# Kernel tuning notes

Hardware: AMD Instinct MI355X
Metric: run time of the kernel (lower is better)

Reference implementation:

```python
import jax, jax.numpy as jnp
import numpy as np

T, B, S, V = 50, 64, 400, 50000
D = 512; E = 512; H = 512; A = 512; POOL = 2


def setup_inputs() -> dict:
    key = jax.random.key(0)
    ks = jax.random.split(key, 20)
    def rn(k, shape, s=0.05):
        return jax.random.normal(k, shape, jnp.float32) * s
    return {
        "input_y": jax.random.randint(ks[0], (T, B), 0, V),
        "hidden": rn(ks[1], (1, B, H), 1.0),
        "context": rn(ks[2], (S, B, E), 1.0),
        "src_pad_mask": jnp.zeros((B, S), jnp.float32),
        "init_att": rn(ks[3], (B, E), 1.0),
        "coverage": jnp.zeros((B, S), jnp.float32),
        "global_ctx": rn(ks[4], (B, E), 1.0),
        "emb_W": rn(ks[5], (V, D)).at[0].set(0.0),  # padding_idx=0
        "W_ih": rn(ks[6], (3 * H, D + E)),
        "W_hh": rn(ks[7], (3 * H, H)),
        "b_ih": jnp.zeros((3 * H,), jnp.float32),
        "b_hh": jnp.zeros((3 * H,), jnp.float32),
        "W_pre": rn(ks[8], (E, A)),
        "b_pre": jnp.zeros((A,), jnp.float32),
        "W_q": rn(ks[9], (H + E, A)),
        "W_v": rn(ks[10], (A,)),
        "W_cov": rn(ks[11], (A,)),
        "W_pgen": rn(ks[12], (E + H + D,)),
        "b_pgen": jnp.zeros((), jnp.float32),
        "W_ro": rn(ks[13], (D + H + E + E, H)),
        "b_ro": jnp.zeros((H,), jnp.float32),
    }


def _gru_cell(x, h, W_ih, W_hh, b_ih, b_hh):
    # PyTorch GRUCell gate order: r, z, n
    gi = x @ W_ih.T + b_ih
    gh = h @ W_hh.T + b_hh
    i_r, i_z, i_n = jnp.split(gi, 3, axis=-1)
    h_r, h_z, h_n = jnp.split(gh, 3, axis=-1)
    r = jax.nn.sigmoid(i_r + h_r)
    z = jax.nn.sigmoid(i_z + h_z)
    n = jnp.tanh(i_n + r * h_n)
    return (1.0 - z) * n + z * h


def reference(input_y, hidden, context, src_pad_mask, init_att, coverage, global_ctx,
              emb_W, W_ih, W_hh, b_ih, b_hh, W_pre, b_pre, W_q, W_v, W_cov,
              W_pgen, b_pgen, W_ro, b_ro):
    emb = emb_W[input_y]                      # [T,B,D]
    ctx = jnp.transpose(context, (1, 0, 2))   # [B,S,E]
    precompute = ctx @ W_pre + b_pre          # [B,S,A] (computed once, as in module)
    pad = src_pad_mask > 0.5
    NEG = jnp.float32(-1e18)

    def step(carry, emb_t):
        h, cur_ctx, cov = carry
        x = jnp.concatenate([emb_t, cur_ctx], 1)          # input feed
        h0 = _gru_cell(x, h[0], W_ih, W_hh, b_ih, b_hh)   # layers=1
        h = h.at[0].set(h0)
        output = h0
        # concat attention with coverage
        q = jnp.concatenate([output, global_ctx], 1) @ W_q          # [B,A]
        tmp = jnp.tanh(precompute + q[:, None, :] + cov[..., None] * W_cov)
        energy = tmp @ W_v                                           # [B,S]
        energy = jnp.where(pad, NEG, energy)
        attn = jax.nn.softmax(energy, axis=1)
        cur_ctx = jnp.einsum('bs,bse->be', attn, ctx)
        # pointer-gen
        p_gen = jax.nn.sigmoid(
            jnp.concatenate([cur_ctx, output, emb_t], 1) @ W_pgen + b_pgen)[:, None]
        # readout + maxout (dropout is identity in eval)
        readout = jnp.concatenate([emb_t, output, cur_ctx, global_ctx], 1) @ W_ro + b_ro
        mo = readout.reshape(B, H // POOL, POOL).max(axis=-1)        # [B,H/POOL]
        cov_loss = jnp.sum(jnp.minimum(attn, cov), 1)                # cov_loss_wt=1.0
        next_cov = cov + attn
        return (h, cur_ctx, next_cov), (mo, p_gen, attn, cov_loss)

    (hidden_f, cur_ctx_f, cov_f), (g_out, g_pg, g_attn, cov_losses) = jax.lax.scan(
        step, (hidden, init_att, coverage), emb)
    return (g_out, hidden_f, g_attn[-1], cur_ctx_f, g_pg, g_attn, cov_losses, cov_f)
```

## Files before the change

### kernel.cpp

```cpp
#include <hip/hip_runtime.h>
#include <hip/hip_bf16.h>


#define T_STEPS 50
#define BB 64
#define SS 400

#define O_GOUT 0
#define O_HID 819200
#define O_ATTN_LAST 851968
#define O_CTXF 877568
#define O_PG 910336
#define O_GATTN 913536
#define O_COVL 2193536
#define O_COVF 2196736

typedef __attribute__((ext_vector_type(4))) float f4;
typedef __attribute__((ext_vector_type(8))) short s8v;
typedef __attribute__((ext_vector_type(4))) unsigned u4;
typedef unsigned long long u64;

static __device__ __forceinline__ float bf2f(unsigned short u){
  unsigned v = ((unsigned)u) << 16; return __builtin_bit_cast(float, v);
}
static __device__ __forceinline__ unsigned short f2bf(float f){
  unsigned u = __builtin_bit_cast(unsigned, f);
  unsigned r = (u + 0x7FFFu + ((u >> 16) & 1u)) >> 16;
  return (unsigned short)r;
}
static __device__ __forceinline__ float sigmoidf_(float x){ return 1.f/(1.f+__expf(-x)); }
static __device__ __forceinline__ float tanhf_(float x){ float e=__expf(2.f*x); return 1.f - 2.f/(e+1.f); }
static __device__ __forceinline__ float ald32f(const float* p){
  unsigned u = __hip_atomic_load((const unsigned*)p, __ATOMIC_RELAXED, __HIP_MEMORY_SCOPE_AGENT);
  return __builtin_bit_cast(float, u);
}
static __device__ __forceinline__ void ast32f(float* p, float v){
  __hip_atomic_store((unsigned*)p, __builtin_bit_cast(unsigned, v),
                     __ATOMIC_RELAXED, __HIP_MEMORY_SCOPE_AGENT);
}
static __device__ __forceinline__ u64 ald64(const void* p){
  return __hip_atomic_load((const u64*)p, __ATOMIC_RELAXED, __HIP_MEMORY_SCOPE_AGENT);
}
static __device__ __forceinline__ void ast64(void* p, u64 v){
  __hip_atomic_store((u64*)p, v, __ATOMIC_RELAXED, __HIP_MEMORY_SCOPE_AGENT);
}

__global__ void conv_ctx(const float* __restrict__ ctx, unsigned short* __restrict__ out){
  int o = blockIdx.x*256 + threadIdx.x;
  if(o >= SS*BB*512) return;
  int e = o & 511; int b = (o>>9)&63; int s = o>>15;
  out[((b*SS+s)<<9) + e] = f2bf(ctx[o]);
}
__global__ void conv_emb(const int* __restrict__ y, const float* __restrict__ embW,
                         unsigned short* __restrict__ embU){
  int o = blockIdx.x*256+threadIdx.x; if(o>=T_STEPS*BB*512) return;
  int d = o & 511; int i = o>>9;
  embU[o] = f2bf(embW[(long)y[i]*512 + d]);
}
__global__ void conv_rest(const float* __restrict__ W_ih, const float* __restrict__ W_hh,
                          const float* __restrict__ W_pre, const float* __restrict__ W_ro,
                          const float* __restrict__ W_q,
                          const float* __restrict__ hidden, const float* __restrict__ init_att,
                          const float* __restrict__ gctx, const float* __restrict__ coverage,
                          unsigned short* __restrict__ wihbf, unsigned short* __restrict__ wpreT,
                          unsigned short* __restrict__ wroT, unsigned short* __restrict__ Wgru,
                          unsigned short* __restrict__ WqP,
                          float* __restrict__ hrow0, unsigned short* __restrict__ h0bf_init,
                          unsigned short* __restrict__ ctx0bf, float* __restrict__ gctxT,
                          float* __restrict__ cov, unsigned* __restrict__ flags){
  int o = blockIdx.x*256+threadIdx.x;
  if(o < 786432){
    int j = o>>9; int d = o&511;
    wihbf[o] = f2bf(W_ih[(long)j*1024 + d]);
  } else if(o < 1048576){
    int p = o - 786432;
    int a = p>>9; int e = p&511;
    wpreT[p] = f2bf(W_pre[(long)e*512 + a]);
  } else if(o < 2097152){
    int p = o - 1048576;
    int n = p>>11; int k = p&2047;
    wroT[p] = f2bf(W_ro[(long)k*512 + n]);
  } else if(o < 3670016){
    int p = o - 2097152;
    int rg = p >> 13; int rem = p & 8191;
    int ki = rem >> 9; int ln = (rem >> 3) & 63; int e = p & 7;
    int blk = rg/24; int r2 = rg%24; int w = r2/6; int r3 = r2%6; int g = r3>>1; int op = r3&1;
    int rl = ln & 15; int kk = ((ln>>4)<<3) + e;
    int d = blk*64 + w*16 + rl; int j = g*512 + d; int k = ki*32 + kk;
    float v = op ? W_hh[(long)j*512 + k] : W_ih[(long)j*1024 + 512 + k];
    Wgru[p] = f2bf(v);
  } else if(o < 3932160){
    int p = o - 3670016;
    int e = p&7; int ln=(p>>3)&63; int kf=(p>>9)&1; int nrg=(p>>10)&31; int blk=p>>15;
    int n = nrg*16 + (ln&15);
    int k = blk*64 + kf*32 + ((ln>>4)<<3) + e;
    WqP[p] = f2bf(W_q[(long)k*512 + n]);
  } else if(o < 4056192){
    int p = o - 3932160;
    if(p < 32768){ float v = hidden[p]; hrow0[p] = v; h0bf_init[p] = f2bf(v); }
    else if(p < 65536){ int q=p-32768; ctx0bf[q] = f2bf(init_att[q]); }
    else if(p < 98304){ int q=p-65536; int b=q>>9,e=q&511; gctxT[e*64+b]=gctx[q]; }
    else if(p < 123904){ int q=p-98304; cov[q]=coverage[q]; }
    else { int q=p-123904; if(q<128) flags[q]=0u; }
  }
}

template<int OUT_BF16>
__global__ __launch_bounds__(256) void mfma_gemm(
    const unsigned short* __restrict__ Abf, int lda,
    const unsigned short* __restrict__ Bbf, int ldb,
    void* __restrict__ Cp, int ldc, const float* __restrict__ bias, int K)
{
  __shared__ __align__(16) unsigned short Ash[128*40];
  __shared__ __align__(16) unsigned short Bsh[128*40];
  int m0 = blockIdx.x*128, n0 = blockIdx.y*128;
  int tid = threadIdx.x;
  int wid = tid>>6, lane = tid&63;
  int wm = wid>>1, wn = wid&1;
  int lr = lane&15, lg = lane>>4;
  f4 acc[4][4];
  #pragma unroll
  for(int i=0;i<4;i++)
    #pragma unroll
    for(int j=0;j<4;j++) acc[i][j]=(f4)0.f;

  for(int kt=0; kt<K; kt+=32){
    #pragma unroll
    for(int c=0;c<2;c++){
      int flat = tid*16 + c*8;
      int row = flat>>5, col = flat&31;
      const unsigned short* ga = Abf + (long)(m0+row)*lda + kt + col;
      *(uint4*)(&Ash[row*40+col]) = *(const uint4*)ga;
      const unsigned short* gb = Bbf + (long)(n0+row)*ldb + kt + col;
      *(uint4*)(&Bsh[row*40+col]) = *(const uint4*)gb;
    }
    __syncthreads();
    s8v av[4], bv[4];
    #pragma unroll
    for(int mi=0;mi<4;mi++) av[mi] = *(const s8v*)(&Ash[(wm*64+mi*16+lr)*40 + lg*8]);
    #pragma unroll
    for(int ni=0;ni<4;ni++) bv[ni] = *(const s8v*)(&Bsh[(wn*64+ni*16+lr)*40 + lg*8]);
    #pragma unroll
    for(int mi=0;mi<4;mi++)
      #pragma unroll
      for(int ni=0;ni<4;ni++)
        acc[mi][ni] = __builtin_amdgcn_mfma_f32_16x16x32_bf16(av[mi], bv[ni], acc[mi][ni], 0,0,0);
    __syncthreads();
  }
  #pragma unroll
  for(int mi=0;mi<4;mi++)
    #pragma unroll
    for(int ni=0;ni<4;ni++){
      int gc = n0 + wn*64 + ni*16 + lr;
      #pragma unroll
      for(int r=0;r<4;r++){
        int gr = m0 + wm*64 + mi*16 + lg*4 + r;
        float v = acc[mi][ni][r];
        if(bias) v += bias[gc];
        if(OUT_BF16) ((unsigned short*)Cp)[(long)gr*ldc + gc] = f2bf(v);
        else         ((float*)Cp)[(long)gr*ldc + gc] = v;
      }
    }
}

__global__ __launch_bounds__(256) void mfma_gemm_ro(
    const unsigned short* __restrict__ embU, const unsigned short* __restrict__ h0bf,
    const unsigned short* __restrict__ ctxA, const unsigned short* __restrict__ wroT,
    float* __restrict__ RO, const float* __restrict__ bias)
{
  __shared__ __align__(16) unsigned short Ash[128*40];
  __shared__ __align__(16) unsigned short Bsh[128*40];
  int m0 = blockIdx.x*128, n0 = blockIdx.y*128;
  int tid = threadIdx.x;
  int wid = tid>>6, lane = tid&63;
  int wm = wid>>1, wn = wid&1;
  int lr = lane&15, lg = lane>>4;
  f4 acc[4][4];
  #pragma unroll
  for(int i=0;i<4;i++)
    #pragma unroll
    for(int j=0;j<4;j++) acc[i][j]=(f4)0.f;

  for(int kt=0; kt<1536; kt+=32){
    const unsigned short* src = (kt<512) ? embU : (kt<1024) ? h0bf : ctxA;
    int klocal = kt & 511;
    #pragma unroll
    for(int c=0;c<2;c++){
      int flat = tid*16 + c*8;
      int row = flat>>5, col = flat&31;
      *(uint4*)(&Ash[row*40+col]) = *(const uint4*)(src + (long)(m0+row)*512 + klocal + col);
      *(uint4*)(&Bsh[row*40+col]) = *(const uint4*)(wroT + (long)(n0+row)*2048 + kt + col);
    }
    __syncthreads();
    s8v av[4], bv[4];
    #pragma unroll
    for(int mi=0;mi<4;mi++) av[mi] = *(const s8v*)(&Ash[(wm*64+mi*16+lr)*40 + lg*8]);
    #pragma unroll
    for(int ni=0;ni<4;ni++) bv[ni] = *(const s8v*)(&Bsh[(wn*64+ni*16+lr)*40 + lg*8]);
    #pragma unroll
    for(int mi=0;mi<4;mi++)
      #pragma unroll
      for(int ni=0;ni<4;ni++)
        acc[mi][ni] = __builtin_amdgcn_mfma_f32_16x16x32_bf16(av[mi], bv[ni], acc[mi][ni], 0,0,0);
    __syncthreads();
  }
  #pragma unroll
  for(int mi=0;mi<4;mi++)
    #pragma unroll
    for(int ni=0;ni<4;ni++){
      int gc = n0 + wn*64 + ni*16 + lr;
      #pragma unroll
      for(int r=0;r<4;r++){
        int gr = m0 + wm*64 + mi*16 + lg*4 + r;
        RO[(long)gr*512 + gc] = acc[mi][ni][r] + bias[gc];
      }
    }
}

__global__ __launch_bounds__(256) void small2(
  const float* __restrict__ AT, const float* __restrict__ W_q, const float* __restrict__ W_ro,
  float* __restrict__ q_g, float* __restrict__ ro_g)
{
  int blk = blockIdx.x;
  int half = blk>>7; int nblk = blk&127;
  int tid = threadIdx.x;
  int b = tid&63; int nq = tid>>6;
  int n = __builtin_amdgcn_readfirstlane(nblk*4 + nq);
  const float* W = half ? W_ro : W_q;
  int koff = half ? 1536 : 512;
  float acc = 0.f;
  const float* wp = W + (long)koff*512 + n;
  #pragma unroll 8
  for(int k=0;k<512;k++){
    acc = fmaf(AT[k*64+b], wp[(long)k*512], acc);
  }
  (half ? ro_g : q_g)[b*512+n] = acc;
}

__global__ __launch_bounds__(512) void k_step(
  const unsigned short* __restrict__ ctx0bf, float* __restrict__ ctxP,
  float* __restrict__ S_part, float* __restrict__ P_exp,
  const unsigned short* __restrict__ hprevbf,
  const float* __restrict__ hrow_in, float* __restrict__ hrow_out,
  const unsigned short* __restrict__ Wp, const unsigned short* __restrict__ WqP,
  const float* __restrict__ gi_emb, const float* __restrict__ b_hh,
  unsigned short* __restrict__ h0bf_all, float* __restrict__ qpart,
  float* __restrict__ cov, unsigned short* __restrict__ ctxA,
  unsigned short* __restrict__ ctxR,
  const unsigned short* __restrict__ pre, const unsigned short* __restrict__ ctxbf,
  const float* __restrict__ q_g, const float* __restrict__ Wv,
  const float* __restrict__ Wcov, const float* __restrict__ padm,
  float* __restrict__ covl_part, unsigned* __restrict__ flags,
  float* __restrict__ outp, int t)
{
  __shared__ __align__(16) char smem[75008];
  const int blk = blockIdx.x;
  const int tid = threadIdx.x;
  const int w = tid>>6, lane = tid&63;
  const int lr = lane&15, lg = lane>>4;

  if(blk < 64){
    if(t==0) return;
    int b = blk; int tb = t-1;
    if(tid < 128){
      const float* Sp = S_part + (tb&1)*256 + b*4;
      float inv = 1.f/(Sp[0]+Sp[1]+Sp[2]+Sp[3]);
      int e0 = tid*4;
      const float* cp = ctxP + (long)b*2048 + e0;
      f4 p0 = *(const f4*)cp;
      f4 p1 = *(const f4*)(cp+512);
      f4 p2 = *(const f4*)(cp+1024);
      f4 p3 = *(const f4*)(cp+1536);
      f4 s = (p0+p1+p2+p3)*inv;
      u64 v = (u64)f2bf(s.x) | ((u64)f2bf(s.y)<<16) | ((u64)f2bf(s.z)<<32) | ((u64)f2bf(s.w)<<48);
      ast64(ctxR + b*512 + e0, v);
      *(u64*)(ctxA + (long)(tb*64+b)*512 + e0) = v;
    }
    asm volatile("s_waitcnt vmcnt(0)" ::: "memory");
    __syncthreads();
    if(tid==0)
      __hip_atomic_fetch_add(flags+64+t, 1u, __ATOMIC_RELEASE, __HIP_MEMORY_SCOPE_AGENT);
    return;
  }

  if(blk < 72){
    int gblk = blk - 64;
    unsigned short* Ash = (unsigned short*)smem;
    unsigned short* HS  = (unsigned short*)(smem+65536);
    const int swz = (lr&7)<<4;
    const int dg = w&3, bh = w>>2;
    const int rgbase = gblk*24 + dg*6;

    if(t>0){
      if(tid==0){
        unsigned it=0;
        while(__hip_atomic_load(flags+64+t, __ATOMIC_RELAXED, __HIP_MEMORY_SCOPE_AGENT) < 64u){
          __builtin_amdgcn_s_sleep(2);
          if(++it > 20000000u) break;
        }
      }
      __syncthreads();
      asm volatile("" ::: "memory");
    }

    f4 acc2[6][2];
    #pragma unroll
    for(int u=0;u<6;u++)
      #pragma unroll
      for(int mm=0;mm<2;mm++) acc2[u][mm]=(f4)0.f;

    for(int kp=0; kp<2; kp++){
      for(int c = tid; c < 4096; c += 512){
        int op = c>>11; int row = (c>>5)&63; int kc = c&31;
        int e0 = kp*256 + kc*8;
        u4 v;
        if(op){
          v = *(const u4*)(hprevbf + row*512 + e0);
        } else if(t>0){
          u64 lo = ald64(ctxR + row*512 + e0);
          u64 hi = ald64(ctxR + row*512 + e0 + 4);
          v.x = (unsigned)lo; v.y = (unsigned)(lo>>32);
          v.z = (unsigned)hi; v.w = (unsigned)(hi>>32);
        } else {
          v = *(const u4*)(ctx0bf + row*512 + e0);
        }
        int dst = op*32768 + row*512 + ((kc*16) ^ ((row&7)<<4));
        *(u4*)((char*)Ash + dst) = v;
      }
      __syncthreads();
      {
        #pragma unroll 2
        for(int ktl=0; ktl<256; ktl+=32){
          s8v av[2][2];
          #pragma unroll
          for(int op=0;op<2;op++)
            #pragma unroll
            for(int mm=0;mm<2;mm++){
              int mi = bh*2+mm;
              av[op][mm] = *(const s8v*)((const char*)Ash + op*32768 + (mi*16+lr)*512 + ((ktl*2 + lg*16) ^ swz));
            }
          int ki = kp*8 + (ktl>>5);
          const unsigned short* wb = Wp + (long)rgbase*8192 + ki*512 + lane*8;
          #pragma unroll
          for(int u=0;u<6;u++){
            s8v bv = *(const s8v*)(wb + (long)u*8192);
            #pragma unroll
            for(int mm=0;mm<2;mm++)
              acc2[u][mm] = __builtin_amdgcn_mfma_f32_16x16x32_bf16(av[u&1][mm], bv, acc2[u][mm], 0,0,0);
          }
        }
      }
      __syncthreads();
    }

    {
      int d = gblk*64 + dg*16 + lr;
      float bhr = b_hh[d], bhz = b_hh[512+d], bhn = b_hh[1024+d];
      #pragma unroll
      for(int mm=0;mm<2;mm++){
        int mi = bh*2+mm;
        #pragma unroll
        for(int r=0;r<4;r++){
          int b = mi*16 + lg*4 + r;
          const float* ge = gi_emb + (long)(t*64+b)*1536;
          float g0 = __builtin_nontemporal_load(ge + d);
          float g1 = __builtin_nontemporal_load(ge + 512 + d);
          float g2 = __builtin_nontemporal_load(ge + 1024 + d);
          float rr = sigmoidf_(g0 + bhr + acc2[0][mm][r] + acc2[1][mm][r]);
          float zz = sigmoidf_(g1 + bhz + acc2[2][mm][r] + acc2[3][mm][r]);
          float nn = tanhf_(  g2       + acc2[4][mm][r] + rr*(acc2[5][mm][r] + bhn));
          float hp = hrow_in[b*512 + d];
          float hv = (1.f-zz)*nn + zz*hp;
          hrow_out[b*512+d] = hv;
          unsigned short hb = f2bf(hv);
          h0bf_all[(long)(t*64+b)*512 + d] = hb;
          HS[b*72 + dg*16 + lr] = hb;
          if(t==T_STEPS-1) outp[O_HID + b*512 + d] = hv;
        }
      }
    }
    __syncthreads();
    {
      #pragma unroll
      for(int i=0;i<8;i++){
        f4 accq[2];
        accq[0]=(f4)0.f; accq[1]=(f4)0.f;
        #pragma unroll
        for(int kf=0;kf<2;kf++){
          s8v bv = *(const s8v*)(WqP + ((((long)gblk*32 + (dg*8+i))*2 + kf)*64 + lane)*8);
          #pragma unroll
          for(int mm=0;mm<2;mm++){
            int mi = bh*2+mm;
            s8v av = *(const s8v*)(HS + (mi*16+lr)*72 + kf*32 + lg*8);
            accq[mm] = __builtin_amdgcn_mfma_f32_16x16x32_bf16(av, bv, accq[mm], 0,0,0);
          }
        }
        int n = dg*128 + i*16 + lr;
        #pragma unroll
        for(int mm=0;mm<2;mm++)
          #pragma unroll
          for(int r=0;r<4;r++)
            ast32f(qpart + (long)gblk*32768 + (long)((bh*2+mm)*16+lg*4+r)*512 + n, accq[mm][r]);
      }
    }
    asm volatile("s_waitcnt vmcnt(0)" ::: "memory");
    __syncthreads();
    if(tid==0)
      __hip_atomic_fetch_add(flags+t, 1u, __ATOMIC_RELEASE, __HIP_MEMORY_SCOPE_AGENT);
    return;
  }

  {
    int eb = blk-72; int b = eb>>2, cq = eb&3, c0 = cq*100;
    float* q_sh  = (float*)smem;
    float* wv_sh = (float*)(smem+2048);
    float* wc_sh = (float*)(smem+4096);
    float* covL  = (float*)(smem+6144);
    float* padL  = (float*)(smem+6560);
    float* red   = (float*)(smem+7392);
    float* red2  = (float*)(smem+9440);
    float* pb    = (float*)(smem+9472);

    wv_sh[tid]=Wv[tid]; wc_sh[tid]=Wcov[tid];
    if(tid<100) padL[tid]=padm[b*400+c0+tid];
    float clp = 0.f;
    if(t>0){
      const float* Sp = S_part + ((t-1)&1)*256 + b*4;
      float inv = 1.f/(Sp[0]+Sp[1]+Sp[2]+Sp[3]);
      if(tid<100){
        float p = P_exp[b*400+c0+tid]*inv;
        float co = cov[b*400+c0+tid];
        clp = fminf(p,co);
        float nc = co+p;
        cov[b*400+c0+tid]=nc;
        covL[tid]=nc;
        outp[O_GATTN + (long)(t-1)*25600 + b*400 + c0 + tid] = p;
      }
    } else {
      if(tid<100) covL[tid]=cov[b*400+c0+tid];
    }
    const unsigned short* prow = pre   + (((long)(b*400+c0))<<9) + lane*8;
    const unsigned short* crow = ctxbf + (((long)(b*400+c0))<<9) + lane*8;
    u4 pr[13], cr[13];
    #pragma unroll
    for(int j=0;j<13;j++){
      int i = w + j*8;
      long ro = (long)((i<100)? i : 0) << 9;
      pr[j] = *(const u4*)(prow + ro);
      cr[j] = *(const u4*)(crow + ro);
    }
    red[tid]=clp; __syncthreads();
    for(int o=256;o;o>>=1){ if(tid<o) red[tid]+=red[tid+o]; __syncthreads(); }
    if(t>0 && tid==0) covl_part[(long)(t-1)*256 + b*4+cq] = red[0];
    if(tid==0){
      unsigned it=0;
      while(__hip_atomic_load(flags+t, __ATOMIC_RELAXED, __HIP_MEMORY_SCOPE_AGENT) < 8u){
        __builtin_amdgcn_s_sleep(8);
        if(++it > 20000000u) break;
      }
    }
    __syncthreads();
    asm volatile("" ::: "memory");
    {
      float acc = q_g[b*512+tid];
      #pragma unroll
      for(int p=0;p<8;p++) acc += ald32f(qpart + ((long)p<<15) + b*512 + tid);
      q_sh[tid] = acc;
    }
    __syncthreads();
    float wsum = 0.f;
    float acc8[8];
    #pragma unroll
    for(int j=0;j<8;j++) acc8[j]=0.f;
    #pragma unroll
    for(int j=0;j<13;j++){
      int i = w + j*8;
      if(i<100){
        u4 cur = pr[j];
        const unsigned* uu = (const unsigned*)&cur;
        float cv = covL[i];
        float part = 0.f;
        #pragma unroll
        for(int q4=0;q4<4;q4++){
          int a = lane*8 + q4*2;
          part += wv_sh[a]  * tanhf_(bf2f((unsigned short)(uu[q4]&0xffffu)) + q_sh[a]   + cv*wc_sh[a]);
          part += wv_sh[a+1]* tanhf_(bf2f((unsigned short)(uu[q4]>>16))    + q_sh[a+1] + cv*wc_sh[a+1]);
        }
        #pragma unroll
        for(int off=32;off;off>>=1) part += __shfl_xor(part, off, 64);
        float e = (padL[i]>0.5f) ? -1e18f : part;
        float p = __expf(e);
        if(lane==0) P_exp[b*400+c0+i] = p;
        wsum += p;
        u4 cc = cr[j];
        const unsigned* cu = (const unsigned*)&cc;
        acc8[0] = fmaf(p, bf2f((unsigned short)(cu[0]&0xffffu)), acc8[0]);
        acc8[1] = fmaf(p, bf2f((unsigned short)(cu[0]>>16)),     acc8[1]);
        acc8[2] = fmaf(p, bf2f((unsigned short)(cu[1]&0xffffu)), acc8[2]);
        acc8[3] = fmaf(p, bf2f((unsigned short)(cu[1]>>16)),     acc8[3]);
        acc8[4] = fmaf(p, bf2f((unsigned short)(cu[2]&0xffffu)), acc8[4]);
        acc8[5] = fmaf(p, bf2f((unsigned short)(cu[2]>>16)),     acc8[5]);
        acc8[6] = fmaf(p, bf2f((unsigned short)(cu[3]&0xffffu)), acc8[6]);
        acc8[7] = fmaf(p, bf2f((unsigned short)(cu[3]>>16)),     acc8[7]);
      }
    }
    if(lane==0) red2[w]=wsum;
    __syncthreads();
    if(tid==0)
      S_part[(t&1)*256 + b*4+cq] = red2[0]+red2[1]+red2[2]+red2[3]+red2[4]+red2[5]+red2[6]+red2[7];
    #pragma unroll
    for(int j=0;j<8;j++) pb[w*512 + lane*8+j] = acc8[j];
    __syncthreads();
    {
      float v = pb[tid]+pb[512+tid]+pb[1024+tid]+pb[1536+tid]
               +pb[2048+tid]+pb[2560+tid]+pb[3072+tid]+pb[3584+tid];
      ctxP[((long)b*4+cq)*512 + tid] = v;
    }
  }
}

__global__ __launch_bounds__(256) void k_fin(
  const float* __restrict__ ctxP, const float* __restrict__ S_part,
  const float* __restrict__ P_exp, const float* __restrict__ cov,
  const float* __restrict__ covl_part,
  unsigned short* __restrict__ ctxA, float* __restrict__ outp)
{
  __shared__ float red[256];
  int b = blockIdx.x; int tid = threadIdx.x;
  const int tb = T_STEPS-1;
  const float* Sp = S_part + 256 + b*4;
  float S = Sp[0]+Sp[1]+Sp[2]+Sp[3];
  float inv = 1.f/S;
  float clp;
  {
    float p = P_exp[b*400+tid]*inv;
    float co = cov[b*400+tid];
    clp = fminf(p, co);
    float nc = co+p;
    outp[O_GATTN + (long)tb*25600 + b*400 + tid] = p;
    outp[O_ATTN_LAST + b*400 + tid] = p;
    outp[O_COVF + b*400 + tid] = nc;
  }
  if(tid<144){
    int i = 256+tid;
    float p = P_exp[b*400+i]*inv;
    float co = cov[b*400+i];
    clp += fminf(p, co);
    float nc = co+p;
    outp[O_GATTN + (long)tb*25600 + b*400 + i] = p;
    outp[O_ATTN_LAST + b*400 + i] = p;
    outp[O_COVF + b*400 + i] = nc;
  }
  red[tid]=clp; __syncthreads();
  for(int o=128;o;o>>=1){ if(tid<o) red[tid]+=red[tid+o]; __syncthreads(); }
  if(tid==0) outp[O_COVL + tb*64 + b] = red[0];
  if(tid<49){
    const float* cp = covl_part + (long)tid*256 + b*4;
    outp[O_COVL + tid*64 + b] = cp[0]+cp[1]+cp[2]+cp[3];
  }
  for(int c=tid;c<512;c+=256){
    float v = (ctxP[(long)b*2048+c]+ctxP[(long)b*2048+512+c]
              +ctxP[(long)b*2048+1024+c]+ctxP[(long)b*2048+1536+c])*inv;
    outp[O_CTXF + b*512 + c] = v;
    ctxA[(long)(tb*64+b)*512 + c] = f2bf(v);
  }
}

__global__ __launch_bounds__(256) void k_post(
  const unsigned short* __restrict__ embU, const unsigned short* __restrict__ h0bf,
  const unsigned short* __restrict__ ctxA, const float* __restrict__ Wpg,
  const float* __restrict__ bpg, const float* __restrict__ RO,
  const float* __restrict__ ro_g, float* __restrict__ outp)
{
  int blk = blockIdx.x;
  if(blk < 800){
    int wid = threadIdx.x>>6, lane=threadIdx.x&63;
    int m = blk*4 + wid;
    float acc=0.f;
    #pragma unroll
    for(int i=0;i<8;i++){
      int k = i*64+lane;
      acc = fmaf(bf2f(ctxA[(long)m*512+k]), Wpg[k], acc);
      acc = fmaf(bf2f(h0bf[(long)m*512+k]), Wpg[512+k], acc);
      acc = fmaf(bf2f(embU[(long)m*512+k]), Wpg[1024+k], acc);
    }
    #pragma unroll
    for(int off=32; off; off>>=1) acc += __shfl_xor(acc, off, 64);
    if(lane==0) outp[O_PG + m] = sigmoidf_(acc + bpg[0]);
  } else {
    int o = (blk-800)*256 + threadIdx.x;
    int h = o & 255; int m = o>>8; int b = m & 63;
    float v0 = RO[(long)m*512 + 2*h]   + ro_g[b*512 + 2*h];
    float v1 = RO[(long)m*512 + 2*h+1] + ro_g[b*512 + 2*h+1];
    outp[O_GOUT + o] = fmaxf(v0,v1);
  }
}

extern "C" void kernel_launch(void* const* d_in, const int* in_sizes, int n_in,
                              void* d_out, int out_size, void* d_ws, size_t ws_size,
                              hipStream_t stream)
{
  (void)in_sizes; (void)n_in; (void)out_size; (void)ws_size;
  const int*   y       = (const int*)d_in[0];
  const float* hidden  = (const float*)d_in[1];
  const float* context = (const float*)d_in[2];
  const float* padm    = (const float*)d_in[3];
  const float* init_att= (const float*)d_in[4];
  const float* coverage= (const float*)d_in[5];
  const float* gctx    = (const float*)d_in[6];
  const float* embW    = (const float*)d_in[7];
  const float* W_ih    = (const float*)d_in[8];
  const float* W_hh    = (const float*)d_in[9];
  const float* b_ih    = (const float*)d_in[10];
  const float* b_hh    = (const float*)d_in[11];
  const float* W_pre   = (const float*)d_in[12];
  const float* b_pre   = (const float*)d_in[13];
  const float* W_q     = (const float*)d_in[14];
  const float* W_v     = (const float*)d_in[15];
  const float* W_cov   = (const float*)d_in[16];
  const float* W_pg    = (const float*)d_in[17];
  const float* b_pg    = (const float*)d_in[18];
  const float* W_ro    = (const float*)d_in[19];
  const float* b_ro    = (const float*)d_in[20];
  float* out = (float*)d_out;

  char* wsb = (char*)d_ws;
  size_t off = 0;
  auto alloc = [&](size_t bytes)->char*{ char* p = wsb+off; off += (bytes+255)&~255UL; return p; };
  unsigned short* pre    = (unsigned short*)alloc(25600UL*512*2);
  unsigned short* ctxbf  = (unsigned short*)alloc(13107200UL*2);
  unsigned short* embU   = (unsigned short*)alloc(3200UL*512*2);
  unsigned short* wihbf  = (unsigned short*)alloc(1536UL*512*2);
  unsigned short* wpreT  = (unsigned short*)alloc(512UL*512*2);
  unsigned short* wroT   = (unsigned short*)alloc(512UL*2048*2);
  unsigned short* Wgru   = (unsigned short*)alloc(192UL*8192*2);
  unsigned short* WqP    = (unsigned short*)alloc(262144UL*2);
  float* gi_emb = (float*)alloc(3200UL*1536*4);
  float* RO     = (float*)alloc(3200UL*512*4);
  float* q_g    = (float*)alloc(64UL*512*4);
  float* ro_g   = (float*)alloc(64UL*512*4);
  float* hrow0  = (float*)alloc(64UL*512*4);
  float* hrow1  = (float*)alloc(64UL*512*4);
  float* gctxT  = (float*)alloc(512UL*64*4);
  unsigned short* h0bf = (unsigned short*)alloc(3200UL*512*2);
  unsigned short* h0bf_init = (unsigned short*)alloc(64UL*512*2);
  unsigned short* ctx0bf    = (unsigned short*)alloc(64UL*512*2);
  unsigned short* ctxA = (unsigned short*)alloc(3200UL*512*2);
  unsigned short* ctxR = (unsigned short*)alloc(64UL*512*2);
  float* ctxP   = (float*)alloc(64UL*4*512*4);
  float* P_exp  = (float*)alloc(64UL*400*4);
  float* S_part = (float*)alloc(2UL*256*4);
  float* qpart  = (float*)alloc(8UL*64*512*4);
  float* cov    = (float*)alloc(64UL*400*4);
  float* covl_part = (float*)alloc(50UL*256*4);
  unsigned* flags = (unsigned*)alloc(128UL*4);

  conv_ctx <<<dim3(51200),dim3(256),0,stream>>>(context, ctxbf);
  conv_emb <<<dim3(6400), dim3(256),0,stream>>>(y, embW, embU);
  conv_rest<<<dim3(15845),dim3(256),0,stream>>>(W_ih, W_hh, W_pre, W_ro, W_q,
                                                hidden, init_att, gctx, coverage,
                                                wihbf, wpreT, wroT, Wgru, WqP,
                                                hrow0, h0bf_init, ctx0bf, gctxT, cov, flags);

  mfma_gemm<1><<<dim3(200,4),dim3(256),0,stream>>>(ctxbf,512, wpreT,512,  pre,   512, b_pre, 512);
  mfma_gemm<0><<<dim3(25,12),dim3(256),0,stream>>>(embU, 512, wihbf,512,  gi_emb,1536, b_ih, 512);
  small2<<<dim3(256),dim3(256),0,stream>>>(gctxT, W_q, W_ro, q_g, ro_g);

  for(int t=0; t<T_STEPS; t++){
    float* hin  = (t&1) ? hrow1 : hrow0;
    float* hout = (t&1) ? hrow0 : hrow1;
    const unsigned short* hprevbf = t ? (h0bf + (long)(t-1)*32768) : h0bf_init;
    k_step<<<dim3(328),dim3(512),0,stream>>>(ctx0bf, ctxP, S_part, P_exp, hprevbf,
                                             hin, hout, Wgru, WqP, gi_emb, b_hh,
                                             h0bf, qpart, cov, ctxA, ctxR, pre, ctxbf,
                                             q_g, W_v, W_cov, padm, covl_part,
                                             flags, out, t);
  }

  k_fin<<<dim3(64),dim3(256),0,stream>>>(ctxP, S_part, P_exp, cov, covl_part, ctxA, out);
  mfma_gemm_ro<<<dim3(25,4),dim3(256),0,stream>>>(embU, h0bf, ctxA, wroT, RO, b_ro);
  k_post<<<dim3(4000),dim3(256),0,stream>>>(embU, h0bf, ctxA, W_pg, b_pg, RO, ro_g, out);
}
```

Before: 2.759 ms.

## Precompute next step's hidden-state GRU GEMM after publishing h, off critical path

The GRU blocks now split the recurrent GEMM. The W_hh·h part for step t+1 is computed at the end of step t, right after all 8 GRU blocks have published h through a new exchange buffer hX. It is stored in gh_buf, so at step t+1 only the context-dependent W_ih·ctx half has to run after waiting on the attention context. This takes about half the GRU matmul work off the critical dependency on the previous step's attention. It adds an inter-block spin wait among the GRU blocks and extra global traffic. Separately, the three conversion kernels are merged into one launch.

```diff
diff --git a/kernel.cpp b/kernel.cpp
--- a/kernel.cpp
+++ b/kernel.cpp
@@ -45,30 +45,33 @@
   __hip_atomic_store((u64*)p, v, __ATOMIC_RELAXED, __HIP_MEMORY_SCOPE_AGENT);
 }
 
-__global__ void conv_ctx(const float* __restrict__ ctx, unsigned short* __restrict__ out){
+__global__ void conv_all(const float* __restrict__ ctx, const int* __restrict__ y,
+                         const float* __restrict__ embW,
+                         const float* __restrict__ W_ih, const float* __restrict__ W_hh,
+                         const float* __restrict__ W_pre, const float* __restrict__ W_ro,
+                         const float* __restrict__ W_q,
+                         const float* __restrict__ hidden, const float* __restrict__ init_att,
+                         const float* __restrict__ gctx, const float* __restrict__ coverage,
+                         unsigned short* __restrict__ ctxbf, unsigned short* __restrict__ embU,
+                         unsigned short* __restrict__ wihbf, unsigned short* __restrict__ wpreT,
+                         unsigned short* __restrict__ wroT, unsigned short* __restrict__ Wgru,
+                         unsigned short* __restrict__ WqP,
+                         float* __restrict__ hrow0, unsigned short* __restrict__ h0bf_init,
+                         unsigned short* __restrict__ ctx0bf, float* __restrict__ gctxT,
+                         float* __restrict__ cov, unsigned* __restrict__ flags){
   int o = blockIdx.x*256 + threadIdx.x;
-  if(o >= SS*BB*512) return;
-  int e = o & 511; int b = (o>>9)&63; int s = o>>15;
-  out[((b*SS+s)<<9) + e] = f2bf(ctx[o]);
-}
-__global__ void conv_emb(const int* __restrict__ y, const float* __restrict__ embW,
-                         unsigned short* __restrict__ embU){
-  int o = blockIdx.x*256+threadIdx.x; if(o>=T_STEPS*BB*512) return;
-  int d = o & 511; int i = o>>9;
-  embU[o] = f2bf(embW[(long)y[i]*512 + d]);
-}
-__global__ void conv_rest(const float* __restrict__ W_ih, const float* __restrict__ W_hh,
-                          const float* __restrict__ W_pre, const float* __restrict__ W_ro,
-                          const float* __restrict__ W_q,
-                          const float* __restrict__ hidden, const float* __restrict__ init_att,
-                          const float* __restrict__ gctx, const float* __restrict__ coverage,
-                          unsigned short* __restrict__ wihbf, unsigned short* __restrict__ wpreT,
-                          unsigned short* __restrict__ wroT, unsigned short* __restrict__ Wgru,
-                          unsigned short* __restrict__ WqP,
-                          float* __restrict__ hrow0, unsigned short* __restrict__ h0bf_init,
-                          unsigned short* __restrict__ ctx0bf, float* __restrict__ gctxT,
-                          float* __restrict__ cov, unsigned* __restrict__ flags){
-  int o = blockIdx.x*256+threadIdx.x;
+  if(o < 13107200){
+    int e = o & 511; int b = (o>>9)&63; int s = o>>15;
+    ctxbf[((b*SS+s)<<9) + e] = f2bf(ctx[o]);
+    return;
+  }
+  o -= 13107200;
+  if(o < 1638400){
+    int d = o & 511; int i = o>>9;
+    embU[o] = f2bf(embW[(long)y[i]*512 + d]);
+    return;
+  }
+  o -= 1638400;
   if(o < 786432){
     int j = o>>9; int d = o&511;
     wihbf[o] = f2bf(W_ih[(long)j*1024 + d]);
@@ -240,13 +243,14 @@
 __global__ __launch_bounds__(512) void k_step(
   const unsigned short* __restrict__ ctx0bf, float* __restrict__ ctxP,
   float* __restrict__ S_part, float* __restrict__ P_exp,
-  const unsigned short* __restrict__ hprevbf,
+  const unsigned short* __restrict__ h0bf_init,
   const float* __restrict__ hrow_in, float* __restrict__ hrow_out,
   const unsigned short* __restrict__ Wp, const unsigned short* __restrict__ WqP,
   const float* __restrict__ gi_emb, const float* __restrict__ b_hh,
   unsigned short* __restrict__ h0bf_all, float* __restrict__ qpart,
   float* __restrict__ cov, unsigned short* __restrict__ ctxA,
-  unsigned short* __restrict__ ctxR,
+  unsigned short* __restrict__ ctxR, unsigned short* __restrict__ hX,
+  float* __restrict__ gh_buf,
   const unsigned short* __restrict__ pre, const unsigned short* __restrict__ ctxbf,
   const float* __restrict__ q_g, const float* __restrict__ Wv,
   const float* __restrict__ Wcov, const float* __restrict__ padm,
@@ -287,48 +291,26 @@
     int gblk = blk - 64;
     unsigned short* Ash = (unsigned short*)smem;
     unsigned short* HS  = (unsigned short*)(smem+65536);
+    char* ash_b = (char*)Ash;
     const int swz = (lr&7)<<4;
     const int dg = w&3, bh = w>>2;
     const int rgbase = gblk*24 + dg*6;
-
-    if(t>0){
-      if(tid==0){
-        unsigned it=0;
-        while(__hip_atomic_load(flags+64+t, __ATOMIC_RELAXED, __HIP_MEMORY_SCOPE_AGENT) < 64u){
-          __builtin_amdgcn_s_sleep(2);
-          if(++it > 20000000u) break;
-        }
-      }
-      __syncthreads();
-      asm volatile("" ::: "memory");
-    }
-
-    f4 acc2[6][2];
-    #pragma unroll
-    for(int u=0;u<6;u++)
-      #pragma unroll
-      for(int mm=0;mm<2;mm++) acc2[u][mm]=(f4)0.f;
-
-    for(int kp=0; kp<2; kp++){
-      for(int c = tid; c < 4096; c += 512){
-        int op = c>>11; int row = (c>>5)&63; int kc = c&31;
-        int e0 = kp*256 + kc*8;
-        u4 v;
-        if(op){
-          v = *(const u4*)(hprevbf + row*512 + e0);
-        } else if(t>0){
-          u64 lo = ald64(ctxR + row*512 + e0);
-          u64 hi = ald64(ctxR + row*512 + e0 + 4);
-          v.x = (unsigned)lo; v.y = (unsigned)(lo>>32);
-          v.z = (unsigned)hi; v.w = (unsigned)(hi>>32);
-        } else {
-          v = *(const u4*)(ctx0bf + row*512 + e0);
-        }
-        int dst = op*32768 + row*512 + ((kc*16) ^ ((row&7)<<4));
-        *(u4*)((char*)Ash + dst) = v;
-      }
-      __syncthreads();
-      {
+    const int d = gblk*64 + dg*16 + lr;
+
+    if(t==0){
+      f4 acc2[6][2];
+      #pragma unroll
+      for(int u=0;u<6;u++){ acc2[u][0]=(f4)0.f; acc2[u][1]=(f4)0.f; }
+      for(int kp=0; kp<2; kp++){
+        for(int c = tid; c < 4096; c += 512){
+          int op = c>>11; int row = (c>>5)&63; int kc = c&31;
+          int e0 = kp*256 + kc*8;
+          u4 v = op ? *(const u4*)(h0bf_init + row*512 + e0)
+                    : *(const u4*)(ctx0bf + row*512 + e0);
+          int dst = op*32768 + row*512 + ((kc*16) ^ ((row&7)<<4));
+          *(u4*)(ash_b + dst) = v;
+        }
+        __syncthreads();
         #pragma unroll 2
         for(int ktl=0; ktl<256; ktl+=32){
           s8v av[2][2];
@@ -337,7 +319,7 @@
             #pragma unroll
             for(int mm=0;mm<2;mm++){
               int mi = bh*2+mm;
-              av[op][mm] = *(const s8v*)((const char*)Ash + op*32768 + (mi*16+lr)*512 + ((ktl*2 + lg*16) ^ swz));
+              av[op][mm] = *(const s8v*)(ash_b + op*32768 + (mi*16+lr)*512 + ((ktl*2 + lg*16) ^ swz));
             }
           int ki = kp*8 + (ktl>>5);
           const unsigned short* wb = Wp + (long)rgbase*8192 + ki*512 + lane*8;
@@ -349,37 +331,95 @@
               acc2[u][mm] = __builtin_amdgcn_mfma_f32_16x16x32_bf16(av[u&1][mm], bv, acc2[u][mm], 0,0,0);
           }
         }
+        __syncthreads();
+      }
+      float bhr = b_hh[d], bhz = b_hh[512+d], bhn = b_hh[1024+d];
+      #pragma unroll
+      for(int mm=0;mm<2;mm++){
+        #pragma unroll
+        for(int r=0;r<4;r++){
+          int bb = (bh*2+mm)*16 + lg*4 + r;
+          const float* ge = gi_emb + (long)(t*64+bb)*1536;
+          float rr = sigmoidf_(ge[d]       + bhr + acc2[0][mm][r] + acc2[1][mm][r]);
+          float zz = sigmoidf_(ge[512+d]   + bhz + acc2[2][mm][r] + acc2[3][mm][r]);
+          float nn = tanhf_(  ge[1024+d]         + acc2[4][mm][r] + rr*(acc2[5][mm][r] + bhn));
+          float hp = hrow_in[bb*512 + d];
+          float hv = (1.f-zz)*nn + zz*hp;
+          hrow_out[bb*512+d] = hv;
+          unsigned short hb = f2bf(hv);
+          h0bf_all[(long)(t*64+bb)*512 + d] = hb;
+          HS[bb*72 + dg*16 + lr] = hb;
+        }
+      }
+    } else {
+      if(tid==0){
+        unsigned it=0;
+        while(__hip_atomic_load(flags+64+t, __ATOMIC_RELAXED, __HIP_MEMORY_SCOPE_AGENT) < 64u){
+          __builtin_amdgcn_s_sleep(2);
+          if(++it > 20000000u) break;
+        }
       }
       __syncthreads();
-    }
-
-    {
-      int d = gblk*64 + dg*16 + lr;
-      float bhr = b_hh[d], bhz = b_hh[512+d], bhn = b_hh[1024+d];
+      asm volatile("" ::: "memory");
+      for(int c = tid; c < 4096; c += 512){
+        int row = c>>6, kc = c&63;
+        u64 lo = ald64(ctxR + row*512 + kc*8);
+        u64 hi = ald64(ctxR + row*512 + kc*8 + 4);
+        u4 v; v.x=(unsigned)lo; v.y=(unsigned)(lo>>32); v.z=(unsigned)hi; v.w=(unsigned)(hi>>32);
+        int dst = row*1024 + ((kc*16) ^ ((row&7)<<4));
+        *(u4*)(ash_b + dst) = v;
+      }
+      __syncthreads();
+      f4 accc[3][2];
+      #pragma unroll
+      for(int g=0;g<3;g++){ accc[g][0]=(f4)0.f; accc[g][1]=(f4)0.f; }
+      #pragma unroll 2
+      for(int kt=0; kt<512; kt+=32){
+        s8v av[2];
+        #pragma unroll
+        for(int mm=0;mm<2;mm++){
+          int mi = bh*2+mm;
+          av[mm] = *(const s8v*)(ash_b + (mi*16+lr)*1024 + ((kt*2 + lg*16) ^ swz));
+        }
+        int ki = kt>>5;
+        const unsigned short* wb = Wp + (long)rgbase*8192 + ki*512 + lane*8;
+        #pragma unroll
+        for(int g=0;g<3;g++){
+          s8v bv = *(const s8v*)(wb + (long)(g*2)*8192);
+          #pragma unroll
+          for(int mm=0;mm<2;mm++)
+            accc[g][mm] = __builtin_amdgcn_mfma_f32_16x16x32_bf16(av[mm], bv, accc[g][mm], 0,0,0);
+        }
+      }
+      __syncthreads();
       #pragma unroll
       for(int mm=0;mm<2;mm++){
-        int mi = bh*2+mm;
         #pragma unroll
         for(int r=0;r<4;r++){
-          int b = mi*16 + lg*4 + r;
-          const float* ge = gi_emb + (long)(t*64+b)*1536;
-          float g0 = __builtin_nontemporal_load(ge + d);
-          float g1 = __builtin_nontemporal_load(ge + 512 + d);
-          float g2 = __builtin_nontemporal_load(ge + 1024 + d);
-          float rr = sigmoidf_(g0 + bhr + acc2[0][mm][r] + acc2[1][mm][r]);
-          float zz = sigmoidf_(g1 + bhz + acc2[2][mm][r] + acc2[3][mm][r]);
-          float nn = tanhf_(  g2       + acc2[4][mm][r] + rr*(acc2[5][mm][r] + bhn));
-          float hp = hrow_in[b*512 + d];
+          int bb = (bh*2+mm)*16 + lg*4 + r;
+          const float* ge = gi_emb + (long)(t*64+bb)*1536;
+          float gh0 = gh_buf[          bb*512 + d];
+          float gh1 = gh_buf[32768 +   bb*512 + d];
+          float gh2 = gh_buf[65536 +   bb*512 + d];
+          float rr = sigmoidf_(ge[d]      + accc[0][mm][r] + gh0);
+          float zz = sigmoidf_(ge[512+d]  + accc[1][mm][r] + gh1);
+          float nn = tanhf_(  ge[1024+d]  + accc[2][mm][r] + rr*gh2);
+          float hp = hrow_in[bb*512 + d];
           float hv = (1.f-zz)*nn + zz*hp;
-          hrow_out[b*512+d] = hv;
+          hrow_out[bb*512+d] = hv;
           unsigned short hb = f2bf(hv);
-          h0bf_all[(long)(t*64+b)*512 + d] = hb;
-          HS[b*72 + dg*16 + lr] = hb;
-          if(t==T_STEPS-1) outp[O_HID + b*512 + d] = hv;
-        }
-      }
-    }
-    __syncthreads();
+          h0bf_all[(long)(t*64+bb)*512 + d] = hb;
+          HS[bb*72 + dg*16 + lr] = hb;
+          if(t==T_STEPS-1) outp[O_HID + bb*512 + d] = hv;
+        }
+      }
+    }
+    __syncthreads();
+    for(int c=tid;c<1024;c+=512){
+      int bb=c>>4, d8=c&15;
+      u64 v = *(const u64*)(HS + bb*72 + d8*4);
+      ast64(hX + bb*512 + gblk*64 + d8*4, v);
+    }
     {
       #pragma unroll
       for(int i=0;i<8;i++){
@@ -407,6 +447,59 @@
     __syncthreads();
     if(tid==0)
       __hip_atomic_fetch_add(flags+t, 1u, __ATOMIC_RELEASE, __HIP_MEMORY_SCOPE_AGENT);
+
+    if(t < T_STEPS-1){
+      if(tid==0){
+        unsigned it=0;
+        while(__hip_atomic_load(flags+t, __ATOMIC_RELAXED, __HIP_MEMORY_SCOPE_AGENT) < 8u){
+          __builtin_amdgcn_s_sleep(2);
+          if(++it > 20000000u) break;
+        }
+      }
+      __syncthreads();
+      asm volatile("" ::: "memory");
+      for(int c = tid; c < 4096; c += 512){
+        int row = c>>6, kc = c&63;
+        u64 lo = ald64(hX + row*512 + kc*8);
+        u64 hi = ald64(hX + row*512 + kc*8 + 4);
+        u4 v; v.x=(unsigned)lo; v.y=(unsigned)(lo>>32); v.z=(unsigned)hi; v.w=(unsigned)(hi>>32);
+        int dst = row*1024 + ((kc*16) ^ ((row&7)<<4));
+        *(u4*)(ash_b + dst) = v;
+      }
+      __syncthreads();
+      f4 acch[3][2];
+      #pragma unroll
+      for(int g=0;g<3;g++){ acch[g][0]=(f4)0.f; acch[g][1]=(f4)0.f; }
+      #pragma unroll 2
+      for(int kt=0; kt<512; kt+=32){
+        s8v av[2];
+        #pragma unroll
+        for(int mm=0;mm<2;mm++){
+          int mi = bh*2+mm;
+          av[mm] = *(const s8v*)(ash_b + (mi*16+lr)*1024 + ((kt*2 + lg*16) ^ swz));
+        }
+        int ki = kt>>5;
+        const unsigned short* wb = Wp + (long)rgbase*8192 + ki*512 + lane*8;
+        #pragma unroll
+        for(int g=0;g<3;g++){
+          s8v bv = *(const s8v*)(wb + (long)(g*2+1)*8192);
+          #pragma unroll
+          for(int mm=0;mm<2;mm++)
+            acch[g][mm] = __builtin_amdgcn_mfma_f32_16x16x32_bf16(av[mm], bv, acch[g][mm], 0,0,0);
+        }
+      }
+      float bhr = b_hh[d], bhz = b_hh[512+d], bhn = b_hh[1024+d];
+      #pragma unroll
+      for(int mm=0;mm<2;mm++){
+        #pragma unroll
+        for(int r=0;r<4;r++){
+          int bb = (bh*2+mm)*16 + lg*4 + r;
+          gh_buf[          bb*512 + d] = acch[0][mm][r] + bhr;
+          gh_buf[32768 +   bb*512 + d] = acch[1][mm][r] + bhz;
+          gh_buf[65536 +   bb*512 + d] = acch[2][mm][r] + bhn;
+        }
+      }
+    }
     return;
   }
 
@@ -647,6 +740,8 @@
   unsigned short* ctx0bf    = (unsigned short*)alloc(64UL*512*2);
   unsigned short* ctxA = (unsigned short*)alloc(3200UL*512*2);
   unsigned short* ctxR = (unsigned short*)alloc(64UL*512*2);
+  unsigned short* hX   = (unsigned short*)alloc(64UL*512*2);
+  float* gh_buf = (float*)alloc(3UL*64*512*4);
   float* ctxP   = (float*)alloc(64UL*4*512*4);
   float* P_exp  = (float*)alloc(64UL*400*4);
   float* S_part = (float*)alloc(2UL*256*4);
@@ -655,12 +750,10 @@
   float* covl_part = (float*)alloc(50UL*256*4);
   unsigned* flags = (unsigned*)alloc(128UL*4);
 
-  conv_ctx <<<dim3(51200),dim3(256),0,stream>>>(context, ctxbf);
-  conv_emb <<<dim3(6400), dim3(256),0,stream>>>(y, embW, embU);
-  conv_rest<<<dim3(15845),dim3(256),0,stream>>>(W_ih, W_hh, W_pre, W_ro, W_q,
-                                                hidden, init_att, gctx, coverage,
-                                                wihbf, wpreT, wroT, Wgru, WqP,
-                                                hrow0, h0bf_init, ctx0bf, gctxT, cov, flags);
+  conv_all<<<dim3(73460),dim3(256),0,stream>>>(context, y, embW, W_ih, W_hh, W_pre, W_ro, W_q,
+                                               hidden, init_att, gctx, coverage,
+                                               ctxbf, embU, wihbf, wpreT, wroT, Wgru, WqP,
+                                               hrow0, h0bf_init, ctx0bf, gctxT, cov, flags);
 
   mfma_gemm<1><<<dim3(200,4),dim3(256),0,stream>>>(ctxbf,512, wpreT,512,  pre,   512, b_pre, 512);
   mfma_gemm<0><<<dim3(25,12),dim3(256),0,stream>>>(embU, 512, wihbf,512,  gi_emb,1536, b_ih, 512);
@@ -669,12 +762,11 @@
   for(int t=0; t<T_STEPS; t++){
     float* hin  = (t&1) ? hrow1 : hrow0;
     float* hout = (t&1) ? hrow0 : hrow1;
-    const unsigned short* hprevbf = t ? (h0bf + (long)(t-1)*32768) : h0bf_init;
-    k_step<<<dim3(328),dim3(512),0,stream>>>(ctx0bf, ctxP, S_part, P_exp, hprevbf,
+    k_step<<<dim3(328),dim3(512),0,stream>>>(ctx0bf, ctxP, S_part, P_exp, h0bf_init,
                                              hin, hout, Wgru, WqP, gi_emb, b_hh,
-                                             h0bf, qpart, cov, ctxA, ctxR, pre, ctxbf,
-                                             q_g, W_v, W_cov, padm, covl_part,
-                                             flags, out, t);
+                                             h0bf, qpart, cov, ctxA, ctxR, hX, gh_buf,
+                                             pre, ctxbf, q_g, W_v, W_cov, padm,
+                                             covl_part, flags, out, t);
   }
 
   k_fin<<<dim3(64),dim3(256),0,stream>>>(ctxP, S_part, P_exp, cov, covl_part, ctxA, out);
```

Result: no change. 2.797 ms (+1.4%).

## Spread inter-block flags across slots and merge conversion kernels into one

Applied to the files above, without the earlier changes.

Replaces the single contended atomic counter per step with per-group flag slots (16 per step). Producers now atomically add or store into separate addresses, and one wavefront polls eight slots in parallel with a vote. The three preprocessing conversion kernels are merged into one launch, and the prefetched attention rows are pinned in registers with empty asm. The goal is less atomic contention and lower handoff latency in the per-step producer/consumer chain, plus fewer launches. The cost is a larger flag array and more polling loads.

```diff
diff --git a/kernel.cpp b/kernel.cpp
--- a/kernel.cpp
+++ b/kernel.cpp
@@ -44,31 +44,35 @@
 static __device__ __forceinline__ void ast64(void* p, u64 v){
   __hip_atomic_store((u64*)p, v, __ATOMIC_RELAXED, __HIP_MEMORY_SCOPE_AGENT);
 }
-
-__global__ void conv_ctx(const float* __restrict__ ctx, unsigned short* __restrict__ out){
+#define PINU4(v) asm volatile("" : "+v"(v.x), "+v"(v.y), "+v"(v.z), "+v"(v.w))
+
+__global__ void conv_all(const float* __restrict__ ctx, const int* __restrict__ y,
+                         const float* __restrict__ embW,
+                         const float* __restrict__ W_ih, const float* __restrict__ W_hh,
+                         const float* __restrict__ W_pre, const float* __restrict__ W_ro,
+                         const float* __restrict__ W_q,
+                         const float* __restrict__ hidden, const float* __restrict__ init_att,
+                         const float* __restrict__ gctx, const float* __restrict__ coverage,
+                         unsigned short* __restrict__ ctxbf, unsigned short* __restrict__ embU,
+                         unsigned short* __restrict__ wihbf, unsigned short* __restrict__ wpreT,
+                         unsigned short* __restrict__ wroT, unsigned short* __restrict__ Wgru,
+                         unsigned short* __restrict__ WqP,
+                         float* __restrict__ hrow0, unsigned short* __restrict__ h0bf_init,
+                         unsigned short* __restrict__ ctx0bf, float* __restrict__ gctxT,
+                         float* __restrict__ cov, unsigned* __restrict__ flags){
   int o = blockIdx.x*256 + threadIdx.x;
-  if(o >= SS*BB*512) return;
-  int e = o & 511; int b = (o>>9)&63; int s = o>>15;
-  out[((b*SS+s)<<9) + e] = f2bf(ctx[o]);
-}
-__global__ void conv_emb(const int* __restrict__ y, const float* __restrict__ embW,
-                         unsigned short* __restrict__ embU){
-  int o = blockIdx.x*256+threadIdx.x; if(o>=T_STEPS*BB*512) return;
-  int d = o & 511; int i = o>>9;
-  embU[o] = f2bf(embW[(long)y[i]*512 + d]);
-}
-__global__ void conv_rest(const float* __restrict__ W_ih, const float* __restrict__ W_hh,
-                          const float* __restrict__ W_pre, const float* __restrict__ W_ro,
-                          const float* __restrict__ W_q,
-                          const float* __restrict__ hidden, const float* __restrict__ init_att,
-                          const float* __restrict__ gctx, const float* __restrict__ coverage,
-                          unsigned short* __restrict__ wihbf, unsigned short* __restrict__ wpreT,
-                          unsigned short* __restrict__ wroT, unsigned short* __restrict__ Wgru,
-                          unsigned short* __restrict__ WqP,
-                          float* __restrict__ hrow0, unsigned short* __restrict__ h0bf_init,
-                          unsigned short* __restrict__ ctx0bf, float* __restrict__ gctxT,
-                          float* __restrict__ cov, unsigned* __restrict__ flags){
-  int o = blockIdx.x*256+threadIdx.x;
+  if(o < 13107200){
+    int e = o & 511; int b = (o>>9)&63; int s = o>>15;
+    ctxbf[((b*SS+s)<<9) + e] = f2bf(ctx[o]);
+    return;
+  }
+  o -= 13107200;
+  if(o < 1638400){
+    int d = o & 511; int i = o>>9;
+    embU[o] = f2bf(embW[(long)y[i]*512 + d]);
+    return;
+  }
+  o -= 1638400;
   if(o < 786432){
     int j = o>>9; int d = o&511;
     wihbf[o] = f2bf(W_ih[(long)j*1024 + d]);
@@ -95,13 +99,13 @@
     int n = nrg*16 + (ln&15);
     int k = blk*64 + kf*32 + ((ln>>4)<<3) + e;
     WqP[p] = f2bf(W_q[(long)k*512 + n]);
-  } else if(o < 4056192){
+  } else if(o < 4057088){
     int p = o - 3932160;
     if(p < 32768){ float v = hidden[p]; hrow0[p] = v; h0bf_init[p] = f2bf(v); }
     else if(p < 65536){ int q=p-32768; ctx0bf[q] = f2bf(init_att[q]); }
     else if(p < 98304){ int q=p-65536; int b=q>>9,e=q&511; gctxT[e*64+b]=gctx[q]; }
     else if(p < 123904){ int q=p-98304; cov[q]=coverage[q]; }
-    else { int q=p-123904; if(q<128) flags[q]=0u; }
+    else { int q=p-123904; if(q<1024) flags[q]=0u; }
   }
 }
 
@@ -279,7 +283,7 @@
     asm volatile("s_waitcnt vmcnt(0)" ::: "memory");
     __syncthreads();
     if(tid==0)
-      __hip_atomic_fetch_add(flags+64+t, 1u, __ATOMIC_RELEASE, __HIP_MEMORY_SCOPE_AGENT);
+      __hip_atomic_fetch_add(&flags[t*16 + (b>>3)], 1u, __ATOMIC_RELEASE, __HIP_MEMORY_SCOPE_AGENT);
     return;
   }
 
@@ -287,14 +291,20 @@
     int gblk = blk - 64;
     unsigned short* Ash = (unsigned short*)smem;
     unsigned short* HS  = (unsigned short*)(smem+65536);
+    char* ash_b = (char*)Ash;
     const int swz = (lr&7)<<4;
     const int dg = w&3, bh = w>>2;
     const int rgbase = gblk*24 + dg*6;
+    const int d = gblk*64 + dg*16 + lr;
 
     if(t>0){
-      if(tid==0){
+      if(w==0){
         unsigned it=0;
-        while(__hip_atomic_load(flags+64+t, __ATOMIC_RELAXED, __HIP_MEMORY_SCOPE_AGENT) < 64u){
+        for(;;){
+          unsigned vv = (lane<8)
+            ? __hip_atomic_load(&flags[t*16+lane], __ATOMIC_RELAXED, __HIP_MEMORY_SCOPE_AGENT)
+            : 8u;
+          if(__all(vv>=8u)) break;
           __builtin_amdgcn_s_sleep(2);
           if(++it > 20000000u) break;
         }
@@ -305,9 +315,7 @@
 
     f4 acc2[6][2];
     #pragma unroll
-    for(int u=0;u<6;u++)
-      #pragma unroll
-      for(int mm=0;mm<2;mm++) acc2[u][mm]=(f4)0.f;
+    for(int u=0;u<6;u++){ acc2[u][0]=(f4)0.f; acc2[u][1]=(f4)0.f; }
 
     for(int kp=0; kp<2; kp++){
       for(int c = tid; c < 4096; c += 512){
@@ -319,63 +327,58 @@
         } else if(t>0){
           u64 lo = ald64(ctxR + row*512 + e0);
           u64 hi = ald64(ctxR + row*512 + e0 + 4);
-          v.x = (unsigned)lo; v.y = (unsigned)(lo>>32);
-          v.z = (unsigned)hi; v.w = (unsigned)(hi>>32);
+          v.x=(unsigned)lo; v.y=(unsigned)(lo>>32); v.z=(unsigned)hi; v.w=(unsigned)(hi>>32);
         } else {
           v = *(const u4*)(ctx0bf + row*512 + e0);
         }
         int dst = op*32768 + row*512 + ((kc*16) ^ ((row&7)<<4));
-        *(u4*)((char*)Ash + dst) = v;
+        *(u4*)(ash_b + dst) = v;
       }
       __syncthreads();
-      {
-        #pragma unroll 2
-        for(int ktl=0; ktl<256; ktl+=32){
-          s8v av[2][2];
+      #pragma unroll 2
+      for(int ktl=0; ktl<256; ktl+=32){
+        s8v av[2][2];
+        #pragma unroll
+        for(int op=0;op<2;op++)
           #pragma unroll
-          for(int op=0;op<2;op++)
-            #pragma unroll
-            for(int mm=0;mm<2;mm++){
-              int mi = bh*2+mm;
-              av[op][mm] = *(const s8v*)((const char*)Ash + op*32768 + (mi*16+lr)*512 + ((ktl*2 + lg*16) ^ swz));
-            }
-          int ki = kp*8 + (ktl>>5);
-          const unsigned short* wb = Wp + (long)rgbase*8192 + ki*512 + lane*8;
+          for(int mm=0;mm<2;mm++){
+            int mi = bh*2+mm;
+            av[op][mm] = *(const s8v*)(ash_b + op*32768 + (mi*16+lr)*512 + ((ktl*2 + lg*16) ^ swz));
+          }
+        int ki = kp*8 + (ktl>>5);
+        const unsigned short* wb = Wp + (long)rgbase*8192 + ki*512 + lane*8;
+        #pragma unroll
+        for(int u=0;u<6;u++){
+          s8v bv = *(const s8v*)(wb + (long)u*8192);
           #pragma unroll
-          for(int u=0;u<6;u++){
-            s8v bv = *(const s8v*)(wb + (long)u*8192);
-            #pragma unroll
-            for(int mm=0;mm<2;mm++)
-              acc2[u][mm] = __builtin_amdgcn_mfma_f32_16x16x32_bf16(av[u&1][mm], bv, acc2[u][mm], 0,0,0);
-          }
+          for(int mm=0;mm<2;mm++)
+            acc2[u][mm] = __builtin_amdgcn_mfma_f32_16x16x32_bf16(av[u&1][mm], bv, acc2[u][mm], 0,0,0);
         }
       }
       __syncthreads();
     }
 
     {
-      int d = gblk*64 + dg*16 + lr;
       float bhr = b_hh[d], bhz = b_hh[512+d], bhn = b_hh[1024+d];
       #pragma unroll
       for(int mm=0;mm<2;mm++){
-        int mi = bh*2+mm;
         #pragma unroll
         for(int r=0;r<4;r++){
-          int b = mi*16 + lg*4 + r;
-          const float* ge = gi_emb + (long)(t*64+b)*1536;
+          int bb = (bh*2+mm)*16 + lg*4 + r;
+          const float* ge = gi_emb + (long)(t*64+bb)*1536;
           float g0 = __builtin_nontemporal_load(ge + d);
           float g1 = __builtin_nontemporal_load(ge + 512 + d);
           float g2 = __builtin_nontemporal_load(ge + 1024 + d);
           float rr = sigmoidf_(g0 + bhr + acc2[0][mm][r] + acc2[1][mm][r]);
           float zz = sigmoidf_(g1 + bhz + acc2[2][mm][r] + acc2[3][mm][r]);
           float nn = tanhf_(  g2       + acc2[4][mm][r] + rr*(acc2[5][mm][r] + bhn));
-          float hp = hrow_in[b*512 + d];
+          float hp = hrow_in[bb*512 + d];
           float hv = (1.f-zz)*nn + zz*hp;
-          hrow_out[b*512+d] = hv;
+          hrow_out[bb*512+d] = hv;
           unsigned short hb = f2bf(hv);
-          h0bf_all[(long)(t*64+b)*512 + d] = hb;
-          HS[b*72 + dg*16 + lr] = hb;
-          if(t==T_STEPS-1) outp[O_HID + b*512 + d] = hv;
+          h0bf_all[(long)(t*64+bb)*512 + d] = hb;
+          HS[bb*72 + dg*16 + lr] = hb;
+          if(t==T_STEPS-1) outp[O_HID + bb*512 + d] = hv;
         }
       }
     }
@@ -406,7 +409,7 @@
     asm volatile("s_waitcnt vmcnt(0)" ::: "memory");
     __syncthreads();
     if(tid==0)
-      __hip_atomic_fetch_add(flags+t, 1u, __ATOMIC_RELEASE, __HIP_MEMORY_SCOPE_AGENT);
+      __hip_atomic_store(&flags[t*16+8+gblk], 1u, __ATOMIC_RELEASE, __HIP_MEMORY_SCOPE_AGENT);
     return;
   }
 
@@ -449,12 +452,18 @@
       pr[j] = *(const u4*)(prow + ro);
       cr[j] = *(const u4*)(crow + ro);
     }
+    #pragma unroll
+    for(int j=0;j<13;j++){ PINU4(pr[j]); PINU4(cr[j]); }
     red[tid]=clp; __syncthreads();
     for(int o=256;o;o>>=1){ if(tid<o) red[tid]+=red[tid+o]; __syncthreads(); }
     if(t>0 && tid==0) covl_part[(long)(t-1)*256 + b*4+cq] = red[0];
-    if(tid==0){
+    if(w==0){
       unsigned it=0;
-      while(__hip_atomic_load(flags+t, __ATOMIC_RELAXED, __HIP_MEMORY_SCOPE_AGENT) < 8u){
+      for(;;){
+        unsigned vv = (lane<8)
+          ? __hip_atomic_load(&flags[t*16+8+lane], __ATOMIC_RELAXED, __HIP_MEMORY_SCOPE_AGENT)
+          : 1u;
+        if(__all(vv>=1u)) break;
         __builtin_amdgcn_s_sleep(8);
         if(++it > 20000000u) break;
       }
@@ -653,14 +662,12 @@
   float* qpart  = (float*)alloc(8UL*64*512*4);
   float* cov    = (float*)alloc(64UL*400*4);
   float* covl_part = (float*)alloc(50UL*256*4);
-  unsigned* flags = (unsigned*)alloc(128UL*4);
-
-  conv_ctx <<<dim3(51200),dim3(256),0,stream>>>(context, ctxbf);
-  conv_emb <<<dim3(6400), dim3(256),0,stream>>>(y, embW, embU);
-  conv_rest<<<dim3(15845),dim3(256),0,stream>>>(W_ih, W_hh, W_pre, W_ro, W_q,
-                                                hidden, init_att, gctx, coverage,
-                                                wihbf, wpreT, wroT, Wgru, WqP,
-                                                hrow0, h0bf_init, ctx0bf, gctxT, cov, flags);
+  unsigned* flags = (unsigned*)alloc(1024UL*4);
+
+  conv_all<<<dim3(73448),dim3(256),0,stream>>>(context, y, embW, W_ih, W_hh, W_pre, W_ro, W_q,
+                                               hidden, init_att, gctx, coverage,
+                                               ctxbf, embU, wihbf, wpreT, wroT, Wgru, WqP,
+                                               hrow0, h0bf_init, ctx0bf, gctxT, cov, flags);
 
   mfma_gemm<1><<<dim3(200,4),dim3(256),0,stream>>>(ctxbf,512, wpreT,512,  pre,   512, b_pre, 512);
   mfma_gemm<0><<<dim3(25,12),dim3(256),0,stream>>>(embU, 512, wihbf,512,  gi_emb,1536, b_ih, 512);
@@ -672,9 +679,9 @@
     const unsigned short* hprevbf = t ? (h0bf + (long)(t-1)*32768) : h0bf_init;
     k_step<<<dim3(328),dim3(512),0,stream>>>(ctx0bf, ctxP, S_part, P_exp, hprevbf,
                                              hin, hout, Wgru, WqP, gi_emb, b_hh,
-                                             h0bf, qpart, cov, ctxA, ctxR, pre, ctxbf,
-                                             q_g, W_v, W_cov, padm, covl_part,
-                                             flags, out, t);
+                                             h0bf, qpart, cov, ctxA, ctxR,
+                                             pre, ctxbf, q_g, W_v, W_cov, padm,
+                                             covl_part, flags, out, t);
   }
 
   k_fin<<<dim3(64),dim3(256),0,stream>>>(ctxP, S_part, P_exp, cov, covl_part, ctxA, out);
```

Result: no change. 2.801 ms (+1.5%).
